# Optimization experiments

Measured on AMD Instinct MI355X. Metric: run time of the kernel, lower is better.

## Reference

```python
import jax, jax.numpy as jnp
import numpy as np

ENC_DIM, DEC_DIM, ATT_DIM = 2048, 512, 512
B, P = 256, 196


def setup_inputs() -> dict:
    key = jax.random.key(0)
    ks = jax.random.split(key, 8)
    s_e = 1.0 / np.sqrt(ENC_DIM)
    s_d = 1.0 / np.sqrt(DEC_DIM)
    s_a = 1.0 / np.sqrt(ATT_DIM)
    return {
        "enc_feature": jax.random.normal(ks[0], (B, P, ENC_DIM), jnp.float32),
        "dec_hidden": jax.random.normal(ks[1], (B, DEC_DIM), jnp.float32),
        "W_enc": jax.random.uniform(ks[2], (ATT_DIM, ENC_DIM), jnp.float32, -s_e, s_e),
        "b_enc": jax.random.uniform(ks[3], (ATT_DIM,), jnp.float32, -s_e, s_e),
        "W_dec": jax.random.uniform(ks[4], (ATT_DIM, DEC_DIM), jnp.float32, -s_d, s_d),
        "b_dec": jax.random.uniform(ks[5], (ATT_DIM,), jnp.float32, -s_d, s_d),
        "W_full": jax.random.uniform(ks[6], (1, ATT_DIM), jnp.float32, -s_a, s_a),
        "b_full": jax.random.uniform(ks[7], (1,), jnp.float32, -s_a, s_a),
    }


def reference(enc_feature, dec_hidden, W_enc, b_enc, W_dec, b_dec, W_full, b_full):
    # att1: [B, P, A]; att2: [B, A]
    att1 = jnp.einsum('bpe,ae->bpa', enc_feature, W_enc) + b_enc
    att2 = jnp.einsum('bd,ad->ba', dec_hidden, W_dec) + b_dec
    h = jax.nn.relu(att1 + att2[:, None, :])            # [B, P, A]
    att = jnp.einsum('bpa,a->bp', h, W_full[0]) + b_full[0]  # [B, P]
    alpha = jax.nn.softmax(att, axis=1)                 # softmax over pixels
    atten_w_enc = jnp.einsum('bpe,bp->be', enc_feature, alpha)
    return atten_w_enc, alpha
```

## Files before the change

kernel.cpp:

```cpp
#include <hip/hip_runtime.h>
#include <hip/hip_bf16.h>
#include <stdint.h>

#define ENC_DIM 2048
#define DEC_DIM 512
#define ATT_DIM 512
#define BATCH   256
#define PIX     196
#define M_TOTAL (BATCH*PIX)
#define NT      (ENC_DIM/64)

typedef unsigned short u16;
typedef __attribute__((ext_vector_type(8))) short  bf16x8;
typedef __attribute__((ext_vector_type(4))) float  f32x4;

__device__ __forceinline__ void gll16(const void* g, void* l) {
    __builtin_amdgcn_global_load_lds(
        (const __attribute__((address_space(1))) unsigned int*)g,
        (__attribute__((address_space(3))) unsigned int*)l,
        16, 0, 0);
}

union Pack8 {
    uint4 u;
    __hip_bfloat16 h[8];
};

__device__ __forceinline__ uint4 cvt8(float4 a, float4 b) {
    Pack8 p;
    p.h[0] = __float2bfloat16(a.x); p.h[1] = __float2bfloat16(a.y);
    p.h[2] = __float2bfloat16(a.z); p.h[3] = __float2bfloat16(a.w);
    p.h[4] = __float2bfloat16(b.x); p.h[5] = __float2bfloat16(b.y);
    p.h[6] = __float2bfloat16(b.z); p.h[7] = __float2bfloat16(b.w);
    return p.u;
}

__global__ void k_convert(const float* __restrict__ W, u16* __restrict__ Wb) {
    int idx = blockIdx.x * 256 + threadIdx.x;
    const float4* s = (const float4*)W + (size_t)idx * 2;
    ((uint4*)Wb)[idx] = cvt8(s[0], s[1]);
}

__global__ void k_att2(const float* __restrict__ dec, const float* __restrict__ Wd,
                       const float* __restrict__ b_enc, const float* __restrict__ b_dec,
                       float* __restrict__ att2f) {
    int b = blockIdx.x;
    int t = threadIdx.x;
    __shared__ float dec_s[DEC_DIM];
    ((float2*)dec_s)[t] = ((const float2*)(dec + (size_t)b * DEC_DIM))[t];
    __syncthreads();
    #pragma unroll
    for (int rep = 0; rep < 2; ++rep) {
        int a = t + rep * 256;
        const float4* w = (const float4*)(Wd + (size_t)a * DEC_DIM);
        float acc = 0.f;
        #pragma unroll 4
        for (int e = 0; e < DEC_DIM / 4; ++e) {
            float4 wv = w[e];
            float4 dv = ((const float4*)dec_s)[e];
            acc += wv.x * dv.x + wv.y * dv.y + wv.z * dv.z + wv.w * dv.w;
        }
        att2f[(size_t)b * ATT_DIM + a] = acc + b_enc[a] + b_dec[a];
    }
}


#define FENCE  asm volatile("" ::: "memory")
#define LGKM0  asm volatile("s_waitcnt lgkmcnt(0)" ::: "memory")
#define VMC(N) asm volatile("s_waitcnt vmcnt(" #N ")" ::: "memory")
#define SBARF  do { FENCE; __builtin_amdgcn_s_barrier(); FENCE; } while (0)

#define ISSUE_A(KT, F) do { const float* _p = a_src + (size_t)(KT) * 64;               \
    F[0] = *(const float4*)(_p);                                                       \
    F[1] = *(const float4*)(_p + 4);                                                   \
    F[2] = *(const float4*)(_p + (size_t)64 * ENC_DIM);                                \
    F[3] = *(const float4*)(_p + (size_t)64 * ENC_DIM + 4); } while (0)

#define WRITE_A(Q, F) do {                                                             \
    *(uint4*)(&As[Q][aw_off])        = cvt8(F[0], F[1]);                               \
    *(uint4*)(&As[Q][aw_off + 4096]) = cvt8(F[2], F[3]); } while (0)

#define STAGE_B(KT, Q) do { const u16* _b = b_src + (size_t)(KT) * 64;                 \
    _Pragma("unroll") for (int s = 0; s < 8; ++s)                                      \
        gll16(_b + (size_t)s * 64 * ENC_DIM, &Bs[Q][s * 4096 + b_dst]); } while (0)

#define COMPUTE(P) do {                                                                \
    _Pragma("unroll") for (int ks = 0; ks < 2; ++ks) {                                 \
        const int _axo = ks ? axo1 : axo0;                                             \
        bf16x8 af[4], bf[8];                                                           \
        _Pragma("unroll") for (int m = 0; m < 4; ++m)                                  \
            af[m] = *(const bf16x8*)(&As[P][a_row_off + m * 1024 + _axo]);             \
        _Pragma("unroll") for (int n = 0; n < 8; ++n)                                  \
            bf[n] = *(const bf16x8*)(&Bs[P][b_row_off + n * 1024 + _axo]);             \
        __builtin_amdgcn_s_setprio(1);                                                 \
        _Pragma("unroll") for (int m = 0; m < 4; ++m)                                  \
            _Pragma("unroll") for (int n = 0; n < 8; ++n)                              \
                acc[m][n] = __builtin_amdgcn_mfma_f32_16x16x32_bf16(af[m], bf[n], acc[m][n], 0, 0, 0); \
        __builtin_amdgcn_s_setprio(0);                                                 \
    } } while (0)

__global__ void __launch_bounds__(512, 1)
k_gemm(const float* __restrict__ enc, const u16* __restrict__ Wb,
       const float* __restrict__ att2f, const float* __restrict__ Wfull,
       float* __restrict__ att_part) {
    const int mb = blockIdx.x;
    const int t  = threadIdx.x;
    const int lane = t & 63, wave = t >> 6;
    const int wm = wave >> 2, wn = wave & 3;
    const int fr = lane & 15, fq = lane >> 4;

    __shared__ u16 As[2][128 * 64];
    __shared__ u16 Bs[2][512 * 64];

    f32x4 acc[4][8];
    #pragma unroll
    for (int m = 0; m < 4; ++m)
        #pragma unroll
        for (int n = 0; n < 8; ++n)
            acc[m][n] = (f32x4){0.f, 0.f, 0.f, 0.f};

    const int arow  = t >> 3;
    const int aslot = t & 7;
    const float* a_src = enc + (size_t)(mb * 128 + arow) * ENC_DIM + aslot * 8;
    const int aw_off = arow * 64 + ((aslot ^ (arow & 7))) * 8;

    const int brl = lane >> 3, bslot = lane & 7;
    const u16* b_src = Wb + (size_t)(wave * 8 + brl) * ENC_DIM + ((bslot ^ brl)) * 8;
    const int b_dst = (wave * 8) * 64;

    const int r7 = fr & 7;
    const int axo0 = ((fq    ) ^ r7) * 8;
    const int axo1 = ((fq | 4) ^ r7) * 8;
    const int a_row_off = (wm * 64 + fr) * 64;
    const int b_row_off = (wn * 128 + fr) * 64;

    float4 eE[4], eO[4];

    ISSUE_A(0, eE); FENCE;
    STAGE_B(0, 0);
    WRITE_A(0, eE);
    FENCE; ISSUE_A(1, eO);
    VMC(4);
    LGKM0;
    SBARF;

    for (int kt = 0; kt < NT - 2; kt += 2) {
        WRITE_A(1, eO);
        STAGE_B(kt + 1, 1); FENCE;
        ISSUE_A(kt + 2, eE);
        COMPUTE(0);
        VMC(4);
        LGKM0;
        SBARF;
        WRITE_A(0, eE);
        STAGE_B(kt + 2, 0); FENCE;
        ISSUE_A(kt + 3, eO);
        COMPUTE(1);
        VMC(4);
        LGKM0;
        SBARF;
    }

    {
        WRITE_A(1, eO);
        STAGE_B(31, 1);
        COMPUTE(0);
        VMC(0);
        LGKM0;
        SBARF;
    }
    COMPUTE(1);

    const int row_base = mb * 128 + wm * 64 + fq * 4;
    const int col_base = wn * 128 + fr;
    float wf[8];
    #pragma unroll
    for (int n = 0; n < 8; ++n) wf[n] = Wfull[col_base + n * 16];

    #pragma unroll
    for (int m = 0; m < 4; ++m) {
        #pragma unroll
        for (int r = 0; r < 4; ++r) {
            const int grow = row_base + m * 16 + r;
            const int bidx = grow / PIX;
            const float* a2 = att2f + (size_t)bidx * ATT_DIM;
            float ssum = 0.f;
            #pragma unroll
            for (int n = 0; n < 8; ++n) {
                float v = acc[m][n][r] + a2[col_base + n * 16];
                v = fmaxf(v, 0.f);
                ssum += v * wf[n];
            }
            #pragma unroll
            for (int off = 1; off < 16; off <<= 1)
                ssum += __shfl_xor(ssum, off, 64);
            if (fr == 0)
                att_part[(size_t)wn * M_TOTAL + grow] = ssum;
        }
    }
}

__global__ void k_soft(const float* __restrict__ att_part, const float* __restrict__ enc,
                       float* __restrict__ out) {
    const int b  = blockIdx.x >> 1;
    const int ec = blockIdx.x & 1;
    const int t  = threadIdx.x;
    __shared__ float red[256];
    __shared__ float alpha_s[PIX];

    float myatt = -1e30f;
    if (t < PIX) {
        float s = 0.f;
        #pragma unroll
        for (int j = 0; j < 4; ++j) s += att_part[(size_t)j * M_TOTAL + b * PIX + t];
        myatt = s;
    }
    red[t] = myatt;
    __syncthreads();
    for (int o = 128; o > 0; o >>= 1) {
        if (t < o) red[t] = fmaxf(red[t], red[t + o]);
        __syncthreads();
    }
    const float mx = red[0];
    __syncthreads();
    float e = 0.f;
    if (t < PIX) e = __expf(myatt - mx);
    red[t] = e;
    __syncthreads();
    for (int o = 128; o > 0; o >>= 1) {
        if (t < o) red[t] += red[t + o];
        __syncthreads();
    }
    const float inv = 1.f / red[0];
    if (t < PIX) {
        float al = e * inv;
        alpha_s[t] = al;
        if (ec == 0) out[(size_t)BATCH * ENC_DIM + b * PIX + t] = al;
    }
    __syncthreads();

    float4 acc = {0.f, 0.f, 0.f, 0.f};
    const float* ebase = enc + (size_t)b * PIX * ENC_DIM + ec * 1024 + t * 4;
    #pragma unroll 4
    for (int p = 0; p < PIX; ++p) {
        float4 x = *(const float4*)(ebase + (size_t)p * ENC_DIM);
        float a = alpha_s[p];
        acc.x += a * x.x; acc.y += a * x.y; acc.z += a * x.z; acc.w += a * x.w;
    }
    *(float4*)(out + (size_t)b * ENC_DIM + ec * 1024 + t * 4) = acc;
}

extern "C" void kernel_launch(void* const* d_in, const int* in_sizes, int n_in,
                              void* d_out, int out_size, void* d_ws, size_t ws_size,
                              hipStream_t stream) {
    const float* enc    = (const float*)d_in[0];
    const float* dec    = (const float*)d_in[1];
    const float* W_enc  = (const float*)d_in[2];
    const float* b_enc  = (const float*)d_in[3];
    const float* W_dec  = (const float*)d_in[4];
    const float* b_dec  = (const float*)d_in[5];
    const float* W_full = (const float*)d_in[6];

    char* ws = (char*)d_ws;
    u16*   Wb    = (u16*)ws;
    float* att2f = (float*)(ws + 2 * 1024 * 1024);
    float* att_p = (float*)(ws + 2 * 1024 * 1024 + 512 * 1024);

    hipLaunchKernelGGL(k_convert, dim3(512), dim3(256), 0, stream, W_enc, Wb);
    hipLaunchKernelGGL(k_att2,    dim3(256), dim3(256), 0, stream, dec, W_dec, b_enc, b_dec, att2f);
    hipLaunchKernelGGL(k_gemm,    dim3(392), dim3(512), 0, stream, enc, Wb, att2f, W_full, att_p);
    hipLaunchKernelGGL(k_soft,    dim3(512), dim3(256), 0, stream, att_p, enc, (float*)d_out);
}
```

Before: 259.9 us.

## Split k-tile compute into barrier-separated phases interleaving LDS reads and staging

Restructures the GEMM main loop into phases. Each phase first issues the LDS fragment reads for half a k-tile, then writes the A tile and stages the next B tile, then runs the 32 MFMAs between workgroup barriers. The aim is to overlap LDS reads and global-to-LDS staging with MFMA execution and to keep waves in lockstep so that memory and matrix phases alternate across waves. The cost is more barriers per k-tile, plus a rewritten epilogue that handles the last tiles separately.

```diff
diff --git a/kernel.cpp b/kernel.cpp
--- a/kernel.cpp
+++ b/kernel.cpp
@@ -84,20 +84,33 @@
     _Pragma("unroll") for (int s = 0; s < 8; ++s)                                      \
         gll16(_b + (size_t)s * 64 * ENC_DIM, &Bs[Q][s * 4096 + b_dst]); } while (0)
 
-#define COMPUTE(P) do {                                                                \
-    _Pragma("unroll") for (int ks = 0; ks < 2; ++ks) {                                 \
-        const int _axo = ks ? axo1 : axo0;                                             \
-        bf16x8 af[4], bf[8];                                                           \
-        _Pragma("unroll") for (int m = 0; m < 4; ++m)                                  \
-            af[m] = *(const bf16x8*)(&As[P][a_row_off + m * 1024 + _axo]);             \
+#define RDF(P, AXO) do {                                                               \
+    _Pragma("unroll") for (int m = 0; m < 4; ++m)                                      \
+        af[m] = *(const bf16x8*)(&As[P][a_row_off + m * 1024 + (AXO)]);                \
+    _Pragma("unroll") for (int n = 0; n < 8; ++n)                                      \
+        bf[n] = *(const bf16x8*)(&Bs[P][b_row_off + n * 1024 + (AXO)]); } while (0)
+
+#define MMA32 do { __builtin_amdgcn_s_setprio(1);                                      \
+    _Pragma("unroll") for (int m = 0; m < 4; ++m)                                      \
         _Pragma("unroll") for (int n = 0; n < 8; ++n)                                  \
-            bf[n] = *(const bf16x8*)(&Bs[P][b_row_off + n * 1024 + _axo]);             \
-        __builtin_amdgcn_s_setprio(1);                                                 \
-        _Pragma("unroll") for (int m = 0; m < 4; ++m)                                  \
-            _Pragma("unroll") for (int n = 0; n < 8; ++n)                              \
-                acc[m][n] = __builtin_amdgcn_mfma_f32_16x16x32_bf16(af[m], bf[n], acc[m][n], 0, 0, 0); \
-        __builtin_amdgcn_s_setprio(0);                                                 \
-    } } while (0)
+            acc[m][n] = __builtin_amdgcn_mfma_f32_16x16x32_bf16(af[m], bf[n], acc[m][n], 0, 0, 0); \
+    __builtin_amdgcn_s_setprio(0); } while (0)
+
+#define PH0(KT, P, Q, FW, FI) do {                                                     \
+    bf16x8 af[4], bf[8];                                                               \
+    RDF(P, axo0);                                            \
+    WRITE_A(Q, FW);                                    \
+    STAGE_B((KT) + 1, Q); FENCE;                         \
+    ISSUE_A((KT) + 2, FI);                                     \
+    SBARF; LGKM0;                                                                      \
+    MMA32;                                                                             \
+    SBARF; } while (0)
+
+#define PH1(P) do {                                                                    \
+    bf16x8 af[4], bf[8];                                                               \
+    RDF(P, axo1);                                                                      \
+    SBARF; LGKM0;                                                                      \
+    MMA32; } while (0)
 
 __global__ void __launch_bounds__(512, 1)
 k_gemm(const float* __restrict__ enc, const u16* __restrict__ Wb,
@@ -145,31 +158,33 @@
     SBARF;
 
     for (int kt = 0; kt < NT - 2; kt += 2) {
-        WRITE_A(1, eO);
-        STAGE_B(kt + 1, 1); FENCE;
-        ISSUE_A(kt + 2, eE);
-        COMPUTE(0);
-        VMC(4);
-        LGKM0;
-        SBARF;
-        WRITE_A(0, eE);
-        STAGE_B(kt + 2, 0); FENCE;
-        ISSUE_A(kt + 3, eO);
-        COMPUTE(1);
-        VMC(4);
-        LGKM0;
-        SBARF;
+        PH0(kt, 0, 1, eO, eE);
+        PH1(0);
+        VMC(4); SBARF;
+        PH0(kt + 1, 1, 0, eE, eO);
+        PH1(1);
+        VMC(4); SBARF;
     }
 
     {
+        bf16x8 af[4], bf[8];
+        RDF(0, axo0);
         WRITE_A(1, eO);
         STAGE_B(31, 1);
-        COMPUTE(0);
-        VMC(0);
-        LGKM0;
+        SBARF; LGKM0;
+        MMA32;
         SBARF;
     }
-    COMPUTE(1);
+    PH1(0);
+    VMC(0); SBARF;
+    {
+        bf16x8 af[4], bf[8];
+        RDF(1, axo0); LGKM0; MMA32;
+    }
+    {
+        bf16x8 af[4], bf[8];
+        RDF(1, axo1); LGKM0; MMA32;
+    }
 
     const int row_base = mb * 128 + wm * 64 + fq * 4;
     const int col_base = wn * 128 + fr;
```

Measured after the change: 288.7 us. +11.1%, slower.

## Load A tile as 128-wide K groups with 32-float-strided coalesced reads

Applied to the files above, without the earlier changes.

Restructures how the fp32 encoder tile is fetched. Each thread now loads eight float4s covering two K-tiles, with lanes contiguous at 16-byte granularity, instead of two adjacent float4s per K-tile. The loads are converted to bf16 and written as half-slots into the swizzled LDS layout. The main loop is unrolled over pairs of 128-wide groups, and some syncs now wait on vmcnt(0). The aim is better global coalescing, at the cost of more live registers and less prefetch depth at some points.

```diff
diff --git a/kernel.cpp b/kernel.cpp
--- a/kernel.cpp
+++ b/kernel.cpp
@@ -26,12 +26,24 @@
     __hip_bfloat16 h[8];
 };
 
+union Pack4 {
+    uint2 u;
+    __hip_bfloat16 h[4];
+};
+
 __device__ __forceinline__ uint4 cvt8(float4 a, float4 b) {
     Pack8 p;
     p.h[0] = __float2bfloat16(a.x); p.h[1] = __float2bfloat16(a.y);
     p.h[2] = __float2bfloat16(a.z); p.h[3] = __float2bfloat16(a.w);
     p.h[4] = __float2bfloat16(b.x); p.h[5] = __float2bfloat16(b.y);
     p.h[6] = __float2bfloat16(b.z); p.h[7] = __float2bfloat16(b.w);
+    return p.u;
+}
+
+__device__ __forceinline__ uint2 cvt4(float4 a) {
+    Pack4 p;
+    p.h[0] = __float2bfloat16(a.x); p.h[1] = __float2bfloat16(a.y);
+    p.h[2] = __float2bfloat16(a.z); p.h[3] = __float2bfloat16(a.w);
     return p.u;
 }
 
@@ -70,15 +82,21 @@
 #define VMC(N) asm volatile("s_waitcnt vmcnt(" #N ")" ::: "memory")
 #define SBARF  do { FENCE; __builtin_amdgcn_s_barrier(); FENCE; } while (0)
 
-#define ISSUE_A(KT, F) do { const float* _p = a_src + (size_t)(KT) * 64;               \
+#define ISSUE_A(G, F) do { const float* _p = a_src + (size_t)(G) * 128;                \
     F[0] = *(const float4*)(_p);                                                       \
-    F[1] = *(const float4*)(_p + 4);                                                   \
-    F[2] = *(const float4*)(_p + (size_t)64 * ENC_DIM);                                \
-    F[3] = *(const float4*)(_p + (size_t)64 * ENC_DIM + 4); } while (0)
-
-#define WRITE_A(Q, F) do {                                                             \
-    *(uint4*)(&As[Q][aw_off])        = cvt8(F[0], F[1]);                               \
-    *(uint4*)(&As[Q][aw_off + 4096]) = cvt8(F[2], F[3]); } while (0)
+    F[1] = *(const float4*)(_p + 32);                                                  \
+    F[2] = *(const float4*)(_p + 64);                                                  \
+    F[3] = *(const float4*)(_p + 96);                                                  \
+    F[4] = *(const float4*)(_p + (size_t)64 * ENC_DIM);                                \
+    F[5] = *(const float4*)(_p + (size_t)64 * ENC_DIM + 32);                           \
+    F[6] = *(const float4*)(_p + (size_t)64 * ENC_DIM + 64);                           \
+    F[7] = *(const float4*)(_p + (size_t)64 * ENC_DIM + 96); } while (0)
+
+#define WRITE_A(Q, F, TL) do {                                                         \
+    *(uint2*)(&As[Q][awA])        = cvt4(F[2*(TL)]);                                   \
+    *(uint2*)(&As[Q][awB])        = cvt4(F[2*(TL) + 1]);                               \
+    *(uint2*)(&As[Q][awA + 4096]) = cvt4(F[4 + 2*(TL)]);                               \
+    *(uint2*)(&As[Q][awB + 4096]) = cvt4(F[5 + 2*(TL)]); } while (0)
 
 #define STAGE_B(KT, Q) do { const u16* _b = b_src + (size_t)(KT) * 64;                 \
     _Pragma("unroll") for (int s = 0; s < 8; ++s)                                      \
@@ -119,10 +137,12 @@
         for (int n = 0; n < 8; ++n)
             acc[m][n] = (f32x4){0.f, 0.f, 0.f, 0.f};
 
-    const int arow  = t >> 3;
-    const int aslot = t & 7;
-    const float* a_src = enc + (size_t)(mb * 128 + arow) * ENC_DIM + aslot * 8;
-    const int aw_off = arow * 64 + ((aslot ^ (arow & 7))) * 8;
+    const int arow = t >> 3;
+    const int h8   = t & 7;
+    const float* a_src = enc + (size_t)(mb * 128 + arow) * ENC_DIM + h8 * 4;
+    const int r7a = arow & 7, h2 = h8 >> 1, h1 = h8 & 1;
+    const int awA = arow * 64 + ((h2    ) ^ r7a) * 8 + h1 * 4;
+    const int awB = arow * 64 + ((4 + h2) ^ r7a) * 8 + h1 * 4;
 
     const int brl = lane >> 3, bslot = lane & 7;
     const u16* b_src = Wb + (size_t)(wave * 8 + brl) * ENC_DIM + ((bslot ^ brl)) * 8;
@@ -134,42 +154,39 @@
     const int a_row_off = (wm * 64 + fr) * 64;
     const int b_row_off = (wn * 128 + fr) * 64;
 
-    float4 eE[4], eO[4];
-
-    ISSUE_A(0, eE); FENCE;
+    float4 fE[8], fO[8];
+
     STAGE_B(0, 0);
-    WRITE_A(0, eE);
-    FENCE; ISSUE_A(1, eO);
-    VMC(4);
+    ISSUE_A(0, fE); FENCE;
+    WRITE_A(0, fE, 0);
     LGKM0;
     SBARF;
 
-    for (int kt = 0; kt < NT - 2; kt += 2) {
-        WRITE_A(1, eO);
-        STAGE_B(kt + 1, 1); FENCE;
-        ISSUE_A(kt + 2, eE);
+    for (int g = 0; g < 16; g += 2) {
+        WRITE_A(1, fE, 1);
+        STAGE_B(2 * g + 1, 1); FENCE;
+        ISSUE_A(g + 1, fO);
         COMPUTE(0);
-        VMC(4);
-        LGKM0;
+        VMC(8); LGKM0; SBARF;
+        WRITE_A(0, fO, 0);
+        STAGE_B(2 * g + 2, 0);
+        COMPUTE(1);
+        VMC(0); LGKM0; SBARF;
+
+        WRITE_A(1, fO, 1);
+        STAGE_B(2 * g + 3, 1); FENCE;
+        if (g + 2 < 16) ISSUE_A(g + 2, fE);
+        COMPUTE(0);
+        if (g + 2 < 16) { VMC(8); } else { VMC(0); }
+        LGKM0; SBARF;
+        if (g + 2 < 16) {
+            WRITE_A(0, fE, 0);
+            STAGE_B(2 * g + 4, 0);
+        }
+        COMPUTE(1);
+        if (g + 2 < 16) { VMC(0); LGKM0; }
         SBARF;
-        WRITE_A(0, eE);
-        STAGE_B(kt + 2, 0); FENCE;
-        ISSUE_A(kt + 3, eO);
-        COMPUTE(1);
-        VMC(4);
-        LGKM0;
-        SBARF;
-    }
-
-    {
-        WRITE_A(1, eO);
-        STAGE_B(31, 1);
-        COMPUTE(0);
-        VMC(0);
-        LGKM0;
-        SBARF;
-    }
-    COMPUTE(1);
+    }
 
     const int row_base = mb * 128 + wm * 64 + fq * 4;
     const int col_base = wn * 128 + fr;
```

Measured after the change: 357.8 us. 37.7% more time.
